# Performance work log

Measured on AMD Instinct MI355X. Metric: run time of the kernel, lower is better.

## Reference

```python
import jax, jax.numpy as jnp
import numpy as np

B, C, H, W = 2, 128, 64, 64  # in_channels == mlp_dim == 128 (residual requires equality)
MLP = 128


def setup_inputs() -> dict:
    key = jax.random.key(0)
    ks = jax.random.split(key, 12)
    s = 1.0 / np.sqrt(C)
    inp = {
        "x": jax.random.normal(ks[0], (B, C, H, W), jnp.float32),
        "y": jax.random.normal(ks[1], (B, C, H, W), jnp.float32),
        # stacked params for the 4 TransLayers: [4, out, in] weights, [4, out] biases
        "Wq": jax.random.uniform(ks[2], (4, MLP, C), jnp.float32, -s, s),
        "bq": jax.random.uniform(ks[3], (4, MLP), jnp.float32, -s, s),
        "Wk": jax.random.uniform(ks[4], (4, MLP, C), jnp.float32, -s, s),
        "bk": jax.random.uniform(ks[5], (4, MLP), jnp.float32, -s, s),
        "Wv": jax.random.uniform(ks[6], (4, MLP, C), jnp.float32, -s, s),
        "bv": jax.random.uniform(ks[7], (4, MLP), jnp.float32, -s, s),
        "Wo": jax.random.uniform(ks[8], (4, MLP, C), jnp.float32, -s, s),
        "bo": jax.random.uniform(ks[9], (4, MLP), jnp.float32, -s, s),
    }
    return inp


def _conv1x1_relu(x, w, b):
    # x: [B,C,H,W], w: [O,C], b: [O]  -> [B,O,H,W]
    return jax.nn.relu(jnp.einsum('bchw,oc->bohw', x, w) + b[None, :, None, None])


def _trans_layer(x, y, wq, bq, wk, bk, wv, bv, wo, bo):
    Q = _conv1x1_relu(x, wq, bq)  # [B,C,H,W]
    K = _conv1x1_relu(y, wk, bk)
    V = _conv1x1_relu(y, wv, bv)
    b, c, h, w = Q.shape
    n = h * w
    Qf = Q.reshape(b, c, n).transpose(0, 2, 1)  # [B,N,C]
    Kf = K.reshape(b, c, n)                      # [B,C,N]
    Vf = V.reshape(b, c, n).transpose(0, 2, 1)   # [B,N,C]
    attn = jax.nn.softmax(jnp.einsum('bnc,bcm->bnm', Qf, Kf), axis=-1)  # unscaled, [B,N,N]
    wV = jnp.einsum('bnm,bmc->bnc', attn, Vf)    # [B,N,C]
    wV = wV.transpose(0, 2, 1).reshape(b, c, h, w)
    return _conv1x1_relu(wV, wo, bo) + x


def reference(x, y, Wq, bq, Wk, bk, Wv, bv, Wo, bo):
    layer = lambda i, a, b_: _trans_layer(a, b_, Wq[i], bq[i], Wk[i], bk[i],
                                          Wv[i], bv[i], Wo[i], bo[i])
    fuse_xy = layer(0, x, y)
    fuse_yz = layer(1, y, x)
    fuse_xx = layer(2, fuse_xy, fuse_xy)
    fuse_yy = layer(3, fuse_yz, fuse_yz)
    return fuse_xx + fuse_yy
```

## Files before the change

kernel.cpp:

```cpp
#include <hip/hip_runtime.h>
#include <math.h>

#define C 128
#define NSP 4096
#define LOG2E 1.4426950408889634f

typedef __attribute__((ext_vector_type(8))) short short8;
typedef __attribute__((ext_vector_type(4))) float f32x4;

static __device__ __forceinline__ unsigned short f2bf(float f) {
    union { float f; unsigned u; } a; a.f = f;
    unsigned r = a.u + 0x7fffu + ((a.u >> 16) & 1u);
    return (unsigned short)(r >> 16);
}

static __device__ __forceinline__ float bf2f(unsigned short s) {
    union { unsigned u; float f; } a; a.u = (unsigned)s << 16;
    return a.f;
}

static __device__ __forceinline__ unsigned pkbf(float a, float b) {
    union { float f; unsigned u; } ua, ub; ua.f = a; ub.f = b;
    return __builtin_amdgcn_perm(ub.u + 0x8000u, ua.u + 0x8000u, 0x07060302u);
}

static __device__ __forceinline__ float ex2(float x) {
#if __has_builtin(__builtin_amdgcn_exp2f)
    return __builtin_amdgcn_exp2f(x);
#else
    return exp2f(x);
#endif
}

static __device__ __forceinline__ f32x4 mfma16(short8 a, short8 b, f32x4 c) {
    return __builtin_amdgcn_mfma_f32_16x16x32_bf16(a, b, c, 0, 0, 0);
}

static __device__ __forceinline__ void stage_w(const float* __restrict__ W,
                                               unsigned short* __restrict__ Wl, int t,
                                               float scale) {
#pragma unroll
    for (int i = 0; i < 16; i++) {
        int idx = i * 256 + t;
        int o = idx >> 5, c4 = (idx & 31) << 2;
        float4 v = *reinterpret_cast<const float4*>(W + o * C + c4);
        uint2 u;
        u.x = pkbf(v.x * scale, v.y * scale);
        u.y = pkbf(v.z * scale, v.w * scale);
        *reinterpret_cast<uint2*>(&Wl[o * 136 + c4]) = u;
    }
}

static __device__ __forceinline__ void stage_in(const float* __restrict__ In, int n0,
                                                unsigned short* __restrict__ Il, int t) {
#pragma unroll
    for (int i = 0; i < 8; i++) {
        int idx = i * 256 + t;
        int c = idx >> 4, n4 = (idx & 15) << 2;
        float4 v = *reinterpret_cast<const float4*>(In + (size_t)c * NSP + n0 + n4);
        Il[(n4 + 0) * 136 + c] = f2bf(v.x);
        Il[(n4 + 1) * 136 + c] = f2bf(v.y);
        Il[(n4 + 2) * 136 + c] = f2bf(v.z);
        Il[(n4 + 3) * 136 + c] = f2bf(v.w);
    }
}

static __device__ __forceinline__ void stage_nc(const unsigned short* __restrict__ In, int n0,
                                                unsigned short* __restrict__ Il, int t) {
#pragma unroll
    for (int i = 0; i < 4; i++) {
        int idx = i * 256 + t;
        int n = idx >> 4, c8 = (idx & 15) << 3;
        uint4 v = *reinterpret_cast<const uint4*>(In + (size_t)(n0 + n) * C + c8);
        *reinterpret_cast<uint4*>(&Il[n * 136 + c8]) = v;
    }
}

__global__ __launch_bounds__(256)
void qkv_kernel(const float* __restrict__ qs0, const float* __restrict__ qs1,
                const float* __restrict__ kv0, const float* __restrict__ kv1,
                const float* __restrict__ Wq, const float* __restrict__ Wk,
                const float* __restrict__ Wv,
                const float* __restrict__ bq, const float* __restrict__ bk,
                const float* __restrict__ bv,
                int layer_base,
                unsigned short* __restrict__ Qb, unsigned short* __restrict__ Kb,
                unsigned short* __restrict__ Vb)
{
    __shared__ __align__(16) unsigned short Wl[128 * 136];
    __shared__ __align__(16) unsigned short Il[64 * 136];
    const int t = threadIdx.x;
    const int ntile = blockIdx.x, kind = blockIdx.y, jb = blockIdx.z;
    const int job = jb >> 1, b = jb & 1, layer = layer_base + job;
    const float* src = (kind == 0) ? (job ? qs1 : qs0) : (job ? kv1 : kv0);
    const float* In = src + (size_t)b * C * NSP;
    const float* W = ((kind == 0) ? Wq : (kind == 1) ? Wk : Wv) + (size_t)layer * C * C;
    const float* bias = ((kind == 0) ? bq : (kind == 1) ? bk : bv) + layer * C;
    unsigned short* Out = ((kind == 0) ? Qb : (kind == 1) ? Kb : Vb) + (size_t)jb * NSP * C;
    const float scale = (kind == 0) ? LOG2E : 1.0f;
    const int n0 = ntile * 64;

    stage_w(W, Wl, t, scale);
    stage_in(In, n0, Il, t);
    __syncthreads();

    const int lane = t & 63, w = t >> 6, l15 = lane & 15, quad = lane >> 4;

    if (kind <= 1) {
        f32x4 acc[4][2];
#pragma unroll
        for (int nt = 0; nt < 4; nt++)
#pragma unroll
            for (int ot = 0; ot < 2; ot++)
#pragma unroll
                for (int r = 0; r < 4; r++) acc[nt][ot][r] = 0.0f;
#pragma unroll
        for (int ks = 0; ks < 4; ks++) {
            int co = ks * 32 + quad * 8;
            short8 b0 = *reinterpret_cast<const short8*>(&Wl[(w * 32 + l15) * 136 + co]);
            short8 b1 = *reinterpret_cast<const short8*>(&Wl[(w * 32 + 16 + l15) * 136 + co]);
#pragma unroll
            for (int nt = 0; nt < 4; nt++) {
                short8 a = *reinterpret_cast<const short8*>(&Il[(nt * 16 + l15) * 136 + co]);
                acc[nt][0] = mfma16(a, b0, acc[nt][0]);
                acc[nt][1] = mfma16(a, b1, acc[nt][1]);
            }
        }
        float bz0 = bias[w * 32 + l15] * scale;
        float bz1 = bias[w * 32 + 16 + l15] * scale;
#pragma unroll
        for (int nt = 0; nt < 4; nt++)
#pragma unroll
            for (int ot = 0; ot < 2; ot++)
#pragma unroll
                for (int r = 0; r < 4; r++) {
                    float v = fmaxf(acc[nt][ot][r] + (ot ? bz1 : bz0), 0.0f);
                    int n = n0 + nt * 16 + quad * 4 + r;
                    int o = w * 32 + ot * 16 + l15;
                    Out[(size_t)n * C + o] = f2bf(v);
                }
    } else {
        f32x4 acc[2][4];
#pragma unroll
        for (int ot = 0; ot < 2; ot++)
#pragma unroll
            for (int nt = 0; nt < 4; nt++)
#pragma unroll
                for (int r = 0; r < 4; r++) acc[ot][nt][r] = 0.0f;
#pragma unroll
        for (int ks = 0; ks < 4; ks++) {
            int co = ks * 32 + quad * 8;
            short8 a0 = *reinterpret_cast<const short8*>(&Wl[(w * 32 + l15) * 136 + co]);
            short8 a1 = *reinterpret_cast<const short8*>(&Wl[(w * 32 + 16 + l15) * 136 + co]);
#pragma unroll
            for (int nt = 0; nt < 4; nt++) {
                short8 bb = *reinterpret_cast<const short8*>(&Il[(nt * 16 + l15) * 136 + co]);
                acc[0][nt] = mfma16(a0, bb, acc[0][nt]);
                acc[1][nt] = mfma16(a1, bb, acc[1][nt]);
            }
        }
#pragma unroll
        for (int ot = 0; ot < 2; ot++)
#pragma unroll
            for (int r = 0; r < 4; r++) {
                int o = w * 32 + ot * 16 + quad * 4 + r;
                float bz = bias[o];
#pragma unroll
                for (int nt = 0; nt < 4; nt++) {
                    float v = fmaxf(acc[ot][nt][r] + bz, 0.0f);
                    Out[(size_t)o * NSP + n0 + nt * 16 + l15] = f2bf(v);
                }
            }
    }
}

__global__ __launch_bounds__(512)
void attn_kernel(const unsigned short* __restrict__ Qb, const unsigned short* __restrict__ Kb,
                 const unsigned short* __restrict__ Vb, unsigned short* __restrict__ Op,
                 float* __restrict__ Lp, int iters)
{
    __shared__ __align__(16) unsigned short Kl[2][32 * 136];
    __shared__ __align__(16) unsigned short Vl[2][128 * 40];
    __shared__ __align__(16) unsigned short Pw[8 * 32 * 40];
    const int t = threadIdx.x, lane = t & 63, w = t >> 6;
    const int l15 = lane & 15, quad = lane >> 4;
    unsigned short* Pm = &Pw[w * 1280];

    const int ksz = gridDim.z;
    const int nwg = gridDim.x * gridDim.y * ksz;
    const int linear = blockIdx.x + gridDim.x * (blockIdx.y + gridDim.y * blockIdx.z);
    const int cpx = nwg >> 3;
    const int wid = (linear & 7) * cpx + (linear >> 3);
    const int ntile = wid & 15;
    const int r2 = wid >> 4;
    const int jb = r2 / ksz, kc = r2 % ksz;

    const int n0 = ntile * 256 + w * 32;
    const int m_begin = kc * iters * 32;
    const unsigned short* Q = Qb + (size_t)jb * NSP * C;
    const unsigned short* K = Kb + (size_t)jb * NSP * C;
    const unsigned short* V = Vb + (size_t)jb * NSP * C;

    short8 qf[2][4];
#pragma unroll
    for (int nt = 0; nt < 2; nt++)
#pragma unroll
        for (int ks = 0; ks < 4; ks++)
            qf[nt][ks] = *reinterpret_cast<const short8*>(
                Q + (size_t)(n0 + nt * 16 + l15) * C + ks * 32 + quad * 8);

    f32x4 o_acc[8][2];
#pragma unroll
    for (int ct = 0; ct < 8; ct++)
#pragma unroll
        for (int nt = 0; nt < 2; nt++)
#pragma unroll
            for (int r = 0; r < 4; r++) o_acc[ct][nt][r] = 0.0f;
    float L[2] = {0.0f, 0.0f};

    uint4 kreg, vreg;
    const int km_ = t >> 4, kc8_ = (t & 15) << 3;
    const int vc_ = t >> 2, vm8_ = (t & 3) << 3;

#define ATT_LOAD(BLK)                                                                  \
    {                                                                                  \
        int mb_ = m_begin + (BLK) * 32;                                                \
        kreg = *reinterpret_cast<const uint4*>(K + (size_t)(mb_ + km_) * C + kc8_);    \
        vreg = *reinterpret_cast<const uint4*>(V + (size_t)vc_ * NSP + mb_ + vm8_);    \
    }

#define ATT_STORE(BUF)                                                                 \
    {                                                                                  \
        *reinterpret_cast<uint4*>(&Kl[BUF][km_ * 136 + kc8_]) = kreg;                  \
        *reinterpret_cast<uint4*>(&Vl[BUF][vc_ * 40 + vm8_]) = vreg;                   \
    }

    ATT_LOAD(0);
    ATT_STORE(0);
    if (iters > 1) ATT_LOAD(1);
    __syncthreads();

    int cur = 0;
    for (int blk = 0; blk < iters; blk++) {
        const unsigned short* Kc = &Kl[cur][0];
        const unsigned short* Vc = &Vl[cur][0];

        f32x4 s[2][2];
#pragma unroll
        for (int mt = 0; mt < 2; mt++)
#pragma unroll
            for (int nt = 0; nt < 2; nt++)
#pragma unroll
                for (int r = 0; r < 4; r++) s[mt][nt][r] = 0.0f;
        __builtin_amdgcn_s_setprio(1);
#pragma unroll
        for (int ks = 0; ks < 4; ks++) {
            int co = ks * 32 + quad * 8;
            short8 k0 = *reinterpret_cast<const short8*>(&Kc[l15 * 136 + co]);
            short8 k1 = *reinterpret_cast<const short8*>(&Kc[(16 + l15) * 136 + co]);
            s[0][0] = mfma16(k0, qf[0][ks], s[0][0]);
            s[0][1] = mfma16(k0, qf[1][ks], s[0][1]);
            s[1][0] = mfma16(k1, qf[0][ks], s[1][0]);
            s[1][1] = mfma16(k1, qf[1][ks], s[1][1]);
        }
        __builtin_amdgcn_s_setprio(0);

        if (blk + 1 < iters) {
            ATT_STORE(cur ^ 1);
            if (blk + 2 < iters) ATT_LOAD(blk + 2);
        }

#pragma unroll
        for (int nt = 0; nt < 2; nt++) {
            float pv[2][4];
            float ls = 0.0f;
#pragma unroll
            for (int mt = 0; mt < 2; mt++)
#pragma unroll
                for (int r = 0; r < 4; r++) {
                    pv[mt][r] = ex2(s[mt][nt][r]);
                    ls += pv[mt][r];
                }
            L[nt] += ls;
#pragma unroll
            for (int mt = 0; mt < 2; mt++) {
                uint2 u;
                u.x = pkbf(pv[mt][0], pv[mt][1]);
                u.y = pkbf(pv[mt][2], pv[mt][3]);
                *reinterpret_cast<uint2*>(&Pm[(nt * 16 + l15) * 40 + mt * 16 + quad * 4]) = u;
            }
        }
        short8 pf0 = *reinterpret_cast<const short8*>(&Pm[l15 * 40 + quad * 8]);
        short8 pf1 = *reinterpret_cast<const short8*>(&Pm[(16 + l15) * 40 + quad * 8]);
        __builtin_amdgcn_s_setprio(1);
#pragma unroll
        for (int ct = 0; ct < 8; ct++) {
            short8 vf = *reinterpret_cast<const short8*>(&Vc[(ct * 16 + l15) * 40 + quad * 8]);
            o_acc[ct][0] = mfma16(vf, pf0, o_acc[ct][0]);
            o_acc[ct][1] = mfma16(vf, pf1, o_acc[ct][1]);
        }
        __builtin_amdgcn_s_setprio(0);

        __syncthreads();
        cur ^= 1;
    }

#undef ATT_LOAD
#undef ATT_STORE

    const size_t kjb = (size_t)(kc * 4 + jb);
#pragma unroll
    for (int nt = 0; nt < 2; nt++) {
        float Lv = L[nt];
        Lv += __shfl_xor(Lv, 16);
        Lv += __shfl_xor(Lv, 32);
        if (quad == 0) Lp[kjb * NSP + n0 + nt * 16 + l15] = Lv;
    }
    unsigned short* Ob = Op + kjb * NSP * C;
#pragma unroll
    for (int ct = 0; ct < 8; ct++)
#pragma unroll
        for (int nt = 0; nt < 2; nt++) {
            uint2 u;
            u.x = pkbf(o_acc[ct][nt][0], o_acc[ct][nt][1]);
            u.y = pkbf(o_acc[ct][nt][2], o_acc[ct][nt][3]);
            *reinterpret_cast<uint2*>(Ob + (size_t)(n0 + nt * 16 + l15) * C + ct * 16 + quad * 4) = u;
        }
}

__global__ __launch_bounds__(256)
void combine_kernel(unsigned short* __restrict__ Op, const float* __restrict__ Lp, int nks)
{
    int gid = blockIdx.x * 256 + threadIdx.x;
    int c8 = (gid & 15) << 3;
    int n  = (gid >> 4) & 4095;
    int jb = gid >> 16;
    float Ls = 0.0f;
    for (int k = 0; k < nks; k++) Ls += Lp[(size_t)(k * 4 + jb) * NSP + n];
    float o[8];
#pragma unroll
    for (int j = 0; j < 8; j++) o[j] = 0.0f;
    for (int k = 0; k < nks; k++) {
        union { uint4 v; unsigned short s[8]; } u;
        u.v = *reinterpret_cast<const uint4*>(Op + ((size_t)(k * 4 + jb) * NSP + n) * C + c8);
#pragma unroll
        for (int j = 0; j < 8; j++) o[j] += bf2f(u.s[j]);
    }
    float inv = 1.0f / Ls;
    uint4 r;
    r.x = pkbf(o[0] * inv, o[1] * inv);
    r.y = pkbf(o[2] * inv, o[3] * inv);
    r.z = pkbf(o[4] * inv, o[5] * inv);
    r.w = pkbf(o[6] * inv, o[7] * inv);
    *reinterpret_cast<uint4*>(Op + ((size_t)jb * NSP + n) * C + c8) = r;
}

__global__ __launch_bounds__(256)
void proj_kernel(const unsigned short* __restrict__ att, const float* __restrict__ Wo,
                 const float* __restrict__ bo, int layer_base,
                 const float* __restrict__ res0, const float* __restrict__ res1,
                 float* __restrict__ out0, float* __restrict__ out1)
{
    __shared__ __align__(16) unsigned short Wl[128 * 136];
    __shared__ __align__(16) unsigned short Il[64 * 136];
    const int t = threadIdx.x;
    const int ntile = blockIdx.x, jb = blockIdx.y;
    const int job = jb >> 1, b = jb & 1, layer = layer_base + job;
    const unsigned short* In = att + (size_t)jb * NSP * C;
    const float* bias = bo + layer * C;
    const float* res = (job ? res1 : res0) + (size_t)b * C * NSP;
    float* out = (job ? out1 : out0) + (size_t)b * C * NSP;
    const int n0 = ntile * 64;

    stage_w(Wo + (size_t)layer * C * C, Wl, t, 1.0f);
    stage_nc(In, n0, Il, t);
    __syncthreads();

    const int lane = t & 63, w = t >> 6, l15 = lane & 15, quad = lane >> 4;
    f32x4 acc[2][4];
#pragma unroll
    for (int ot = 0; ot < 2; ot++)
#pragma unroll
        for (int nt = 0; nt < 4; nt++)
#pragma unroll
            for (int r = 0; r < 4; r++) acc[ot][nt][r] = 0.0f;
#pragma unroll
    for (int ks = 0; ks < 4; ks++) {
        int co = ks * 32 + quad * 8;
        short8 a0 = *reinterpret_cast<const short8*>(&Wl[(w * 32 + l15) * 136 + co]);
        short8 a1 = *reinterpret_cast<const short8*>(&Wl[(w * 32 + 16 + l15) * 136 + co]);
#pragma unroll
        for (int nt = 0; nt < 4; nt++) {
            short8 bb = *reinterpret_cast<const short8*>(&Il[(nt * 16 + l15) * 136 + co]);
            acc[0][nt] = mfma16(a0, bb, acc[0][nt]);
            acc[1][nt] = mfma16(a1, bb, acc[1][nt]);
        }
    }
#pragma unroll
    for (int ot = 0; ot < 2; ot++)
#pragma unroll
        for (int r = 0; r < 4; r++) {
            int o = w * 32 + ot * 16 + quad * 4 + r;
            float bz = bias[o];
#pragma unroll
            for (int nt = 0; nt < 4; nt++) {
                int n = n0 + nt * 16 + l15;
                float v = fmaxf(acc[ot][nt][r] + bz, 0.0f) + res[(size_t)o * NSP + n];
                out[(size_t)o * NSP + n] = v;
            }
        }
}

__global__ __launch_bounds__(256)
void final_kernel(const unsigned short* __restrict__ att, const float* __restrict__ Wo,
                  const float* __restrict__ bo,
                  const float* __restrict__ fuse0, const float* __restrict__ fuse1,
                  float* __restrict__ out)
{
    __shared__ __align__(16) unsigned short Wl[128 * 136];
    __shared__ __align__(16) unsigned short Il[64 * 136];
    const int t = threadIdx.x;
    const int ntile = blockIdx.x, b = blockIdx.y;
    const int n0 = ntile * 64;
    const int lane = t & 63, w = t >> 6, l15 = lane & 15, quad = lane >> 4;

    float tot[2][4][4];
#pragma unroll
    for (int ot = 0; ot < 2; ot++)
#pragma unroll
        for (int nt = 0; nt < 4; nt++)
#pragma unroll
            for (int r = 0; r < 4; r++) tot[ot][nt][r] = 0.0f;

    for (int j = 0; j < 2; j++) {
        if (j) __syncthreads();
        int layer = 2 + j;
        stage_w(Wo + (size_t)layer * C * C, Wl, t, 1.0f);
        stage_nc(att + (size_t)(j * 2 + b) * NSP * C, n0, Il, t);
        __syncthreads();

        f32x4 acc[2][4];
#pragma unroll
        for (int ot = 0; ot < 2; ot++)
#pragma unroll
            for (int nt = 0; nt < 4; nt++)
#pragma unroll
                for (int r = 0; r < 4; r++) acc[ot][nt][r] = 0.0f;
#pragma unroll
        for (int ks = 0; ks < 4; ks++) {
            int co = ks * 32 + quad * 8;
            short8 a0 = *reinterpret_cast<const short8*>(&Wl[(w * 32 + l15) * 136 + co]);
            short8 a1 = *reinterpret_cast<const short8*>(&Wl[(w * 32 + 16 + l15) * 136 + co]);
#pragma unroll
            for (int nt = 0; nt < 4; nt++) {
                short8 bb = *reinterpret_cast<const short8*>(&Il[(nt * 16 + l15) * 136 + co]);
                acc[0][nt] = mfma16(a0, bb, acc[0][nt]);
                acc[1][nt] = mfma16(a1, bb, acc[1][nt]);
            }
        }
        const float* bias = bo + layer * C;
        const float* fuse = (j ? fuse1 : fuse0) + (size_t)b * C * NSP;
#pragma unroll
        for (int ot = 0; ot < 2; ot++)
#pragma unroll
            for (int r = 0; r < 4; r++) {
                int o = w * 32 + ot * 16 + quad * 4 + r;
                float bz = bias[o];
#pragma unroll
                for (int nt = 0; nt < 4; nt++) {
                    int n = n0 + nt * 16 + l15;
                    tot[ot][nt][r] += fmaxf(acc[ot][nt][r] + bz, 0.0f) + fuse[(size_t)o * NSP + n];
                }
            }
    }
#pragma unroll
    for (int ot = 0; ot < 2; ot++)
#pragma unroll
        for (int r = 0; r < 4; r++) {
            int o = w * 32 + ot * 16 + quad * 4 + r;
#pragma unroll
            for (int nt = 0; nt < 4; nt++) {
                int n = n0 + nt * 16 + l15;
                out[(size_t)b * C * NSP + (size_t)o * NSP + n] = tot[ot][nt][r];
            }
        }
}

extern "C" void kernel_launch(void* const* d_in, const int* in_sizes, int n_in,
                              void* d_out, int out_size, void* d_ws, size_t ws_size,
                              hipStream_t stream)
{
    (void)in_sizes; (void)n_in; (void)out_size;
    const float* x  = (const float*)d_in[0];
    const float* y  = (const float*)d_in[1];
    const float* Wq = (const float*)d_in[2];
    const float* bq = (const float*)d_in[3];
    const float* Wk = (const float*)d_in[4];
    const float* bk = (const float*)d_in[5];
    const float* Wv = (const float*)d_in[6];
    const float* bv = (const float*)d_in[7];
    const float* Wo = (const float*)d_in[8];
    const float* bo = (const float*)d_in[9];
    float* out = (float*)d_out;
    char* ws = (char*)d_ws;

    int ks = (ws_size >= 55050240u) ? 8 : (ws_size >= 38010880u) ? 4 : 2;
    int iters = 128 / ks;

    unsigned short* Qb = (unsigned short*)(ws);
    unsigned short* Kb = (unsigned short*)(ws + (4u << 20));
    unsigned short* Vb = (unsigned short*)(ws + (8u << 20));
    unsigned short* Op = (unsigned short*)(ws + (12u << 20));
    size_t op_bytes = (size_t)ks * 4 * NSP * C * 2;
    float* Lp = (float*)(ws + (12u << 20) + op_bytes);
    float* fuse0 = Lp + (size_t)ks * 4 * NSP;
    float* fuse1 = fuse0 + (size_t)2 * C * NSP;
    unsigned short* att = Op;

    qkv_kernel<<<dim3(64, 3, 4), 256, 0, stream>>>(x, y, y, x, Wq, Wk, Wv, bq, bk, bv, 0,
                                                   Qb, Kb, Vb);
    attn_kernel<<<dim3(16, 4, ks), 512, 0, stream>>>(Qb, Kb, Vb, Op, Lp, iters);
    combine_kernel<<<dim3(1024), 256, 0, stream>>>(Op, Lp, ks);
    proj_kernel<<<dim3(64, 4), 256, 0, stream>>>(att, Wo, bo, 0, x, y, fuse0, fuse1);

    qkv_kernel<<<dim3(64, 3, 4), 256, 0, stream>>>(fuse0, fuse1, fuse0, fuse1, Wq, Wk, Wv,
                                                   bq, bk, bv, 2, Qb, Kb, Vb);
    attn_kernel<<<dim3(16, 4, ks), 512, 0, stream>>>(Qb, Kb, Vb, Op, Lp, iters);
    combine_kernel<<<dim3(1024), 256, 0, stream>>>(Op, Lp, ks);
    final_kernel<<<dim3(64, 2), 256, 0, stream>>>(att, Wo, bo, fuse0, fuse1, out);
}
```

Baseline: 222.1 us.

## Switch attention to 32x32x16 MFMA and keep P in registers via permlane swap

The attention kernel now uses the 32x32x16 bf16 MFMA in place of the 16x16x32 one for both the QK^T scores and the PV accumulation. Because the 32x32 accumulator layout lines up with the B-operand layout after a permlane32 swap, the softmax probabilities are repacked in registers and no longer round-trip through the per-wave LDS scratch buffer. This drops LDS writes and reads, a shared buffer, and some instruction overhead per block. The trade-off is the longer latency of the larger MFMA and new lane-mapping logic that must be correct for the output and row-sum writes.

```diff
diff --git a/kernel.cpp b/kernel.cpp
--- a/kernel.cpp
+++ b/kernel.cpp
@@ -7,6 +7,7 @@
 
 typedef __attribute__((ext_vector_type(8))) short short8;
 typedef __attribute__((ext_vector_type(4))) float f32x4;
+typedef __attribute__((ext_vector_type(16))) float f32x16;
 
 static __device__ __forceinline__ unsigned short f2bf(float f) {
     union { float f; unsigned u; } a; a.f = f;
@@ -34,6 +35,10 @@
 
 static __device__ __forceinline__ f32x4 mfma16(short8 a, short8 b, f32x4 c) {
     return __builtin_amdgcn_mfma_f32_16x16x32_bf16(a, b, c, 0, 0, 0);
+}
+
+static __device__ __forceinline__ f32x16 mfma32(short8 a, short8 b, f32x16 c) {
+    return __builtin_amdgcn_mfma_f32_32x32x16_bf16(a, b, c, 0, 0, 0);
 }
 
 static __device__ __forceinline__ void stage_w(const float* __restrict__ W,
@@ -181,10 +186,8 @@
 {
     __shared__ __align__(16) unsigned short Kl[2][32 * 136];
     __shared__ __align__(16) unsigned short Vl[2][128 * 40];
-    __shared__ __align__(16) unsigned short Pw[8 * 32 * 40];
     const int t = threadIdx.x, lane = t & 63, w = t >> 6;
-    const int l15 = lane & 15, quad = lane >> 4;
-    unsigned short* Pm = &Pw[w * 1280];
+    const int l31 = lane & 31, hi = lane >> 5;
 
     const int ksz = gridDim.z;
     const int nwg = gridDim.x * gridDim.y * ksz;
@@ -201,22 +204,18 @@
     const unsigned short* K = Kb + (size_t)jb * NSP * C;
     const unsigned short* V = Vb + (size_t)jb * NSP * C;
 
-    short8 qf[2][4];
-#pragma unroll
-    for (int nt = 0; nt < 2; nt++)
-#pragma unroll
-        for (int ks = 0; ks < 4; ks++)
-            qf[nt][ks] = *reinterpret_cast<const short8*>(
-                Q + (size_t)(n0 + nt * 16 + l15) * C + ks * 32 + quad * 8);
-
-    f32x4 o_acc[8][2];
-#pragma unroll
-    for (int ct = 0; ct < 8; ct++)
-#pragma unroll
-        for (int nt = 0; nt < 2; nt++)
-#pragma unroll
-            for (int r = 0; r < 4; r++) o_acc[ct][nt][r] = 0.0f;
-    float L[2] = {0.0f, 0.0f};
+    short8 qf[8];
+#pragma unroll
+    for (int ks = 0; ks < 8; ks++)
+        qf[ks] = *reinterpret_cast<const short8*>(
+            Q + (size_t)(n0 + l31) * C + ks * 16 + hi * 8);
+
+    f32x16 o_acc[4];
+#pragma unroll
+    for (int ct = 0; ct < 4; ct++)
+#pragma unroll
+        for (int r = 0; r < 16; r++) o_acc[ct][r] = 0.0f;
+    float L = 0.0f;
 
     uint4 kreg, vreg;
     const int km_ = t >> 4, kc8_ = (t & 15) << 3;
@@ -245,23 +244,14 @@
         const unsigned short* Kc = &Kl[cur][0];
         const unsigned short* Vc = &Vl[cur][0];
 
-        f32x4 s[2][2];
-#pragma unroll
-        for (int mt = 0; mt < 2; mt++)
-#pragma unroll
-            for (int nt = 0; nt < 2; nt++)
-#pragma unroll
-                for (int r = 0; r < 4; r++) s[mt][nt][r] = 0.0f;
+        f32x16 s;
+#pragma unroll
+        for (int r = 0; r < 16; r++) s[r] = 0.0f;
         __builtin_amdgcn_s_setprio(1);
 #pragma unroll
-        for (int ks = 0; ks < 4; ks++) {
-            int co = ks * 32 + quad * 8;
-            short8 k0 = *reinterpret_cast<const short8*>(&Kc[l15 * 136 + co]);
-            short8 k1 = *reinterpret_cast<const short8*>(&Kc[(16 + l15) * 136 + co]);
-            s[0][0] = mfma16(k0, qf[0][ks], s[0][0]);
-            s[0][1] = mfma16(k0, qf[1][ks], s[0][1]);
-            s[1][0] = mfma16(k1, qf[0][ks], s[1][0]);
-            s[1][1] = mfma16(k1, qf[1][ks], s[1][1]);
+        for (int ks = 0; ks < 8; ks++) {
+            short8 ka = *reinterpret_cast<const short8*>(&Kc[l31 * 136 + ks * 16 + hi * 8]);
+            s = mfma32(ka, qf[ks], s);
         }
         __builtin_amdgcn_s_setprio(0);
 
@@ -270,34 +260,34 @@
             if (blk + 2 < iters) ATT_LOAD(blk + 2);
         }
 
-#pragma unroll
-        for (int nt = 0; nt < 2; nt++) {
-            float pv[2][4];
-            float ls = 0.0f;
-#pragma unroll
-            for (int mt = 0; mt < 2; mt++)
-#pragma unroll
-                for (int r = 0; r < 4; r++) {
-                    pv[mt][r] = ex2(s[mt][nt][r]);
-                    ls += pv[mt][r];
-                }
-            L[nt] += ls;
-#pragma unroll
-            for (int mt = 0; mt < 2; mt++) {
-                uint2 u;
-                u.x = pkbf(pv[mt][0], pv[mt][1]);
-                u.y = pkbf(pv[mt][2], pv[mt][3]);
-                *reinterpret_cast<uint2*>(&Pm[(nt * 16 + l15) * 40 + mt * 16 + quad * 4]) = u;
-            }
-        }
-        short8 pf0 = *reinterpret_cast<const short8*>(&Pm[l15 * 40 + quad * 8]);
-        short8 pf1 = *reinterpret_cast<const short8*>(&Pm[(16 + l15) * 40 + quad * 8]);
+        float p[16];
+        float ls = 0.0f;
+#pragma unroll
+        for (int r = 0; r < 16; r++) {
+            p[r] = ex2(s[r]);
+            ls += p[r];
+        }
+        L += ls;
+
+        unsigned a0 = pkbf(p[0], p[1]),  a1 = pkbf(p[2], p[3]);
+        unsigned b0 = pkbf(p[4], p[5]),  b1 = pkbf(p[6], p[7]);
+        unsigned c0 = pkbf(p[8], p[9]),  c1 = pkbf(p[10], p[11]);
+        unsigned d0 = pkbf(p[12], p[13]), d1 = pkbf(p[14], p[15]);
+        asm("v_permlane32_swap_b32 %0, %1" : "+v"(a0), "+v"(b0));
+        asm("v_permlane32_swap_b32 %0, %1" : "+v"(a1), "+v"(b1));
+        asm("v_permlane32_swap_b32 %0, %1" : "+v"(c0), "+v"(d0));
+        asm("v_permlane32_swap_b32 %0, %1" : "+v"(c1), "+v"(d1));
+        union { uint4 u; short8 s8; } f0u, f1u;
+        f0u.u = make_uint4(a0, a1, b0, b1);
+        f1u.u = make_uint4(c0, c1, d0, d1);
+
         __builtin_amdgcn_s_setprio(1);
 #pragma unroll
-        for (int ct = 0; ct < 8; ct++) {
-            short8 vf = *reinterpret_cast<const short8*>(&Vc[(ct * 16 + l15) * 40 + quad * 8]);
-            o_acc[ct][0] = mfma16(vf, pf0, o_acc[ct][0]);
-            o_acc[ct][1] = mfma16(vf, pf1, o_acc[ct][1]);
+        for (int ct = 0; ct < 4; ct++) {
+            short8 v0 = *reinterpret_cast<const short8*>(&Vc[(ct * 32 + l31) * 40 + hi * 8]);
+            short8 v1 = *reinterpret_cast<const short8*>(&Vc[(ct * 32 + l31) * 40 + 16 + hi * 8]);
+            o_acc[ct] = mfma32(v0, f0u.s8, o_acc[ct]);
+            o_acc[ct] = mfma32(v1, f1u.s8, o_acc[ct]);
         }
         __builtin_amdgcn_s_setprio(0);
 
@@ -309,22 +299,21 @@
 #undef ATT_STORE
 
     const size_t kjb = (size_t)(kc * 4 + jb);
-#pragma unroll
-    for (int nt = 0; nt < 2; nt++) {
-        float Lv = L[nt];
-        Lv += __shfl_xor(Lv, 16);
-        Lv += __shfl_xor(Lv, 32);
-        if (quad == 0) Lp[kjb * NSP + n0 + nt * 16 + l15] = Lv;
-    }
+    float Lv = L + __shfl_xor(L, 32);
+    if (lane < 32) Lp[kjb * NSP + n0 + l31] = Lv;
+
     unsigned short* Ob = Op + kjb * NSP * C;
-#pragma unroll
-    for (int ct = 0; ct < 8; ct++)
-#pragma unroll
-        for (int nt = 0; nt < 2; nt++) {
+    const int n = n0 + l31;
+    unsigned short* On = Ob + (size_t)n * C + hi * 4;
+#pragma unroll
+    for (int ct = 0; ct < 4; ct++)
+#pragma unroll
+        for (int rb = 0; rb < 4; rb++) {
+            int r0 = rb * 4;
             uint2 u;
-            u.x = pkbf(o_acc[ct][nt][0], o_acc[ct][nt][1]);
-            u.y = pkbf(o_acc[ct][nt][2], o_acc[ct][nt][3]);
-            *reinterpret_cast<uint2*>(Ob + (size_t)(n0 + nt * 16 + l15) * C + ct * 16 + quad * 4) = u;
+            u.x = pkbf(o_acc[ct][r0 + 0], o_acc[ct][r0 + 1]);
+            u.y = pkbf(o_acc[ct][r0 + 2], o_acc[ct][r0 + 3]);
+            *reinterpret_cast<uint2*>(On + ct * 32 + rb * 8) = u;
         }
 }
 
```

Result: no change. 223.5 us (+0.6%).
